# Kernel optimization log

Hardware: AMD Instinct MI355X
Metric: run time of the kernel (lower is better)

Reference implementation:

```python
import jax, jax.numpy as jnp
import numpy as np

NUM_MIX = 50
CMD_LEN = 4
ARG_LEN = 6
MIX_TEMP = 0.0001
GAUSS_TEMP = 0.0001


def setup_inputs() -> dict:
    key = jax.random.key(0)
    k1, k2, k3 = jax.random.split(key, 3)
    S, B, H = 51, 2048, 1024
    out_ch = CMD_LEN + ARG_LEN * NUM_MIX * 3  # 904
    decoder_output = jax.random.normal(k1, (S, B, H), dtype=jnp.float32)
    W = jax.random.normal(k2, (out_ch, H), dtype=jnp.float32) * (1.0 / np.sqrt(H))
    b = jax.random.normal(k3, (out_ch,), dtype=jnp.float32) * 0.01
    return {"decoder_output": decoder_output, "W": W, "b": b}


def reference(decoder_output, W, b):
    S, B, H = decoder_output.shape
    # fc: [S,B,H] @ [H,out_ch] + b  -> [S,B,904]
    ret = jnp.einsum('sbh,oh->sbo', decoder_output, W) + b

    key = jax.random.key(42)
    k_cmd, k_mix, k_gauss = jax.random.split(key, 3)

    # command: temperature softmax + categorical sample + one-hot
    cmd_logits = ret[..., :CMD_LEN] / MIX_TEMP  # [S,B,4]
    cmd_idx = jax.random.categorical(k_cmd, cmd_logits)  # [S,B]
    command = jax.nn.one_hot(cmd_idx, CMD_LEN, dtype=decoder_output.dtype)

    # MDN coefficients over flattened rows: N = S*B*ARG_LEN
    arguments = ret[..., CMD_LEN:].reshape(-1, 3 * NUM_MIX)  # [N,150]
    logmix = arguments[:, :NUM_MIX]
    mean = arguments[:, NUM_MIX:2 * NUM_MIX]
    logstd = arguments[:, 2 * NUM_MIX:]
    logmix = logmix - jax.nn.logsumexp(logmix, axis=-1, keepdims=True)

    # sample mixture component with temperature (softmax of logmix/temp)
    mix_idx = jax.random.categorical(k_mix, logmix / MIX_TEMP)  # [N]

    # vectorized gather of chosen mean/logstd (replaces per-row python loop)
    chosen_mean = jnp.take_along_axis(mean, mix_idx[:, None], axis=1)[:, 0]
    chosen_logstd = jnp.take_along_axis(logstd, mix_idx[:, None], axis=1)[:, 0]

    noise = jax.random.normal(k_gauss, chosen_mean.shape, dtype=chosen_mean.dtype)
    noise = noise * np.sqrt(GAUSS_TEMP)
    args_out = chosen_mean + jnp.exp(chosen_logstd) * noise  # [N]
    args_out = args_out.reshape(-1, B, ARG_LEN)  # [S,B,6]

    return jnp.concatenate([command, args_out], axis=-1)  # [S,B,10]
```

## Files before the change

### kernel.cpp

```cpp
#include <hip/hip_runtime.h>
#include <stdint.h>
#include <math.h>

#pragma clang fp contract(off)

#define M_TOTAL 104448
#define N_OUT   904
#define K_DIM   1024

#define BM 64
#define BN 64
#define BK 16

typedef float f32x2 __attribute__((ext_vector_type(2)));

__device__ inline f32x2 pk_mul(f32x2 a, f32x2 b) {
    f32x2 d;
    asm("v_pk_mul_f32 %0, %1, %2" : "=v"(d) : "v"(a), "v"(b));
    return d;
}
__device__ inline f32x2 pk_add(f32x2 a, f32x2 b) {
    f32x2 d;
    asm("v_pk_add_f32 %0, %1, %2" : "=v"(d) : "v"(a), "v"(b));
    return d;
}

__host__ __device__ inline uint32_t rotl32(uint32_t x, int r) {
    return (x << r) | (x >> (32 - r));
}

__host__ __device__ inline void threefry2x32(uint32_t k0, uint32_t k1,
                                             uint32_t x0, uint32_t x1,
                                             uint32_t& o0, uint32_t& o1) {
    uint32_t ks2 = k0 ^ k1 ^ 0x1BD11BDAu;
    x0 += k0; x1 += k1;
#define R4(a,b,c,d) \
    x0 += x1; x1 = rotl32(x1,(a)); x1 ^= x0; \
    x0 += x1; x1 = rotl32(x1,(b)); x1 ^= x0; \
    x0 += x1; x1 = rotl32(x1,(c)); x1 ^= x0; \
    x0 += x1; x1 = rotl32(x1,(d)); x1 ^= x0;
    R4(13,15,26,6)  x0 += k1;  x1 += ks2 + 1u;
    R4(17,29,16,24) x0 += ks2; x1 += k0  + 2u;
    R4(13,15,26,6)  x0 += k0;  x1 += k1  + 3u;
    R4(17,29,16,24) x0 += k1;  x1 += ks2 + 4u;
    R4(13,15,26,6)  x0 += ks2; x1 += k0  + 5u;
#undef R4
    o0 = x0; o1 = x1;
}

__device__ inline uint32_t random_bits_part(uint32_t k0, uint32_t k1, uint32_t idx) {
    uint32_t o0, o1;
    threefry2x32(k0, k1, 0u, idx, o0, o1);
    return o0 ^ o1;
}

__device__ inline float bits_to_unit(uint32_t bits) {
    return __uint_as_float((bits >> 9) | 0x3f800000u) - 1.0f;
}

__device__ inline float logf_cr(float x) { return (float)log((double)x); }
__device__ inline float expf_cr(float x) { return (float)exp((double)x); }

__device__ inline float gumbel_at(uint32_t k0, uint32_t k1, uint32_t idx) {
    float f = bits_to_unit(random_bits_part(k0, k1, idx));
    float u = fmaxf(f, 1.17549435e-38f);
    float t = logf_cr(u);
    return -logf_cr(-t);
}

__device__ inline float erfinv_xla(float x) {
    float w = -log1pf(-x * x);
    float p;
    if (w < 5.0f) {
        w = w - 2.5f;
        p = 2.81022636e-08f;
        p = 3.43273939e-07f  + p * w;
        p = -3.5233877e-06f  + p * w;
        p = -4.39150654e-06f + p * w;
        p = 0.00021858087f   + p * w;
        p = -0.00125372503f  + p * w;
        p = -0.00417768164f  + p * w;
        p = 0.246640727f     + p * w;
        p = 1.50140941f      + p * w;
    } else {
        w = sqrtf(w) - 3.0f;
        p = -0.000200214257f;
        p = 0.000100950558f  + p * w;
        p = 0.00134934322f   + p * w;
        p = -0.00367342844f  + p * w;
        p = 0.00573950773f   + p * w;
        p = -0.0076224613f   + p * w;
        p = 0.00943887047f   + p * w;
        p = 1.00167406f      + p * w;
        p = 2.83297682f      + p * w;
    }
    return p * x;
}

__global__ __launch_bounds__(256) void gemm_np_sse_pk2(
    const float* __restrict__ X,
    const float* __restrict__ W,
    const float* __restrict__ bias,
    float* __restrict__ ret,
    int rows)
{
    __shared__ f32x2 As2[8][68];
    __shared__ f32x2 Bs2[8][100];

    const int t  = threadIdx.x;
    const int tx = t & 15;
    const int ty = t >> 4;
    const int m0 = blockIdx.y * BM;
    const int n0 = blockIdx.x * BN;

    const int sm  = t >> 2;
    const int skq = t & 3;
    const int bse = sm + 2 * (sm >> 2);

    const float* Xrow = X + (size_t)(m0 + sm) * K_DIM + skq * 4;
    const float* Wrow = W + (size_t)(n0 + sm) * K_DIM + skq * 4;
    const bool   wok  = (n0 + sm) < N_OUT;

    f32x2 acc[2][4][4];
#pragma unroll
    for (int h = 0; h < 2; h++)
#pragma unroll
        for (int i = 0; i < 4; i++)
#pragma unroll
            for (int j = 0; j < 4; j++) acc[h][i][j] = (f32x2){0.0f, 0.0f};

    float4 av = *(const float4*)(Xrow);
    float4 bv = wok ? *(const float4*)(Wrow) : make_float4(0.f, 0.f, 0.f, 0.f);

    for (int k0 = 0; k0 < K_DIM; k0 += BK) {
        __syncthreads();
        As2[skq * 2 + 0][sm]  = (f32x2){av.x, av.y};
        As2[skq * 2 + 1][sm]  = (f32x2){av.z, av.w};
        Bs2[skq * 2 + 0][bse] = (f32x2){bv.x, bv.y};
        Bs2[skq * 2 + 1][bse] = (f32x2){bv.z, bv.w};
        __syncthreads();

        if (k0 + BK < K_DIM) {
            av = *(const float4*)(Xrow + k0 + BK);
            bv = wok ? *(const float4*)(Wrow + k0 + BK)
                     : make_float4(0.f, 0.f, 0.f, 0.f);
        }

#pragma unroll
        for (int q = 3; q >= 0; q--) {
#pragma unroll
            for (int h = 0; h < 2; h++) {
                const int kp = q * 2 + h;
                float4 aa0 = *(const float4*)&As2[kp][ty * 4];
                float4 aa1 = *(const float4*)&As2[kp][ty * 4 + 2];
                float4 bb0 = *(const float4*)&Bs2[kp][tx * 6];
                float4 bb1 = *(const float4*)&Bs2[kp][tx * 6 + 2];
                f32x2 a0 = {aa0.x, aa0.y}, a1 = {aa0.z, aa0.w};
                f32x2 a2 = {aa1.x, aa1.y}, a3 = {aa1.z, aa1.w};
                f32x2 b0 = {bb0.x, bb0.y}, b1 = {bb0.z, bb0.w};
                f32x2 b2 = {bb1.x, bb1.y}, b3 = {bb1.z, bb1.w};
                acc[h][0][0] = pk_add(pk_mul(a0, b0), acc[h][0][0]);
                acc[h][0][1] = pk_add(pk_mul(a0, b1), acc[h][0][1]);
                acc[h][0][2] = pk_add(pk_mul(a0, b2), acc[h][0][2]);
                acc[h][0][3] = pk_add(pk_mul(a0, b3), acc[h][0][3]);
                acc[h][1][0] = pk_add(pk_mul(a1, b0), acc[h][1][0]);
                acc[h][1][1] = pk_add(pk_mul(a1, b1), acc[h][1][1]);
                acc[h][1][2] = pk_add(pk_mul(a1, b2), acc[h][1][2]);
                acc[h][1][3] = pk_add(pk_mul(a1, b3), acc[h][1][3]);
                acc[h][2][0] = pk_add(pk_mul(a2, b0), acc[h][2][0]);
                acc[h][2][1] = pk_add(pk_mul(a2, b1), acc[h][2][1]);
                acc[h][2][2] = pk_add(pk_mul(a2, b2), acc[h][2][2]);
                acc[h][2][3] = pk_add(pk_mul(a2, b3), acc[h][2][3]);
                acc[h][3][0] = pk_add(pk_mul(a3, b0), acc[h][3][0]);
                acc[h][3][1] = pk_add(pk_mul(a3, b1), acc[h][3][1]);
                acc[h][3][2] = pk_add(pk_mul(a3, b2), acc[h][3][2]);
                acc[h][3][3] = pk_add(pk_mul(a3, b3), acc[h][3][3]);
            }
        }
    }

#pragma unroll
    for (int i = 0; i < 4; i++) {
        int m = m0 + ty * 4 + i;
        if (m >= rows) continue;
#pragma unroll
        for (int j = 0; j < 4; j++) {
            int o = n0 + tx * 4 + j;
            if (o >= N_OUT) continue;
            f32x2 s01 = acc[0][i][j];
            f32x2 s23 = acc[1][i][j];
            float res = (s01.x + s01.y) + (s23.x + s23.y);
            ret[(size_t)m * N_OUT + o] = res + bias[o];
        }
    }
}

__global__ __launch_bounds__(256) void sample_kernel(
    const float* __restrict__ ret,
    float* __restrict__ out,
    int m0_global, int rows,
    uint32_t kc0, uint32_t kc1,
    uint32_t km0, uint32_t km1,
    uint32_t kg0, uint32_t kg1)
{
    const int lane = threadIdx.x & 63;
    const int wid  = threadIdx.x >> 6;
    const int rloc = blockIdx.x * 4 + wid;
    if (rloc >= rows) return;
    const int m = m0_global + rloc;

    const float* r = ret + (size_t)rloc * N_OUT;
    float* o = out + (size_t)m * 10;

    const float LO = __uint_as_float(0xBF7FFFFFu);
    const float SQRT2 = __uint_as_float(0x3FB504F3u);

    {
        float v; int idx = lane;
        if (lane < 4) {
            float g = gumbel_at(kc0, kc1, (uint32_t)(m * 4 + lane));
            v = r[lane] / 0.0001f + g;
        } else {
            v = -INFINITY;
        }
#pragma unroll
        for (int off = 1; off < 64; off <<= 1) {
            float v2 = __shfl_xor(v, off);
            int   i2 = __shfl_xor(idx, off);
            if (v2 > v || (v2 == v && i2 < idx)) { v = v2; idx = i2; }
        }
        if (lane < 4) o[lane] = (lane == idx) ? 1.0f : 0.0f;
    }

    for (int a = 0; a < 6; a++) {
        const float* base = r + 4 + a * 150;
        float l = (lane < 50) ? base[lane] : -INFINITY;

        float mx = l;
#pragma unroll
        for (int off = 1; off < 64; off <<= 1) mx = fmaxf(mx, __shfl_xor(mx, off));

        float e = (lane < 50) ? expf_cr(l - mx) : 0.0f;

        float rj = (lane < 8) ? e : 0.0f;
#pragma unroll
        for (int tstep = 1; tstep <= 5; tstep++) {
            float ev = __shfl(e, (lane & 7) + 8 * tstep);
            if (lane < 8) rj = rj + ev;
        }
        float r0 = __shfl(rj, 0), r1 = __shfl(rj, 1), r2 = __shfl(rj, 2), r3 = __shfl(rj, 3);
        float r4 = __shfl(rj, 4), r5 = __shfl(rj, 5), r6 = __shfl(rj, 6), r7 = __shfl(rj, 7);
        float s = ((r0 + r1) + (r2 + r3)) + ((r4 + r5) + (r6 + r7));
        s = s + __shfl(e, 48);
        s = s + __shfl(e, 49);

        float lse = logf_cr(s) + mx;

        float vv; int ii = lane;
        if (lane < 50) {
            float g = gumbel_at(km0, km1, (uint32_t)((m * 6 + a) * 50 + lane));
            vv = (l - lse) / 0.0001f + g;
        } else {
            vv = -INFINITY;
        }
#pragma unroll
        for (int off = 1; off < 64; off <<= 1) {
            float v2 = __shfl_xor(vv, off);
            int   i2 = __shfl_xor(ii, off);
            if (v2 > vv || (v2 == vv && i2 < ii)) { vv = v2; ii = i2; }
        }

        if (lane == 0) {
            float mean = base[50 + ii];
            float lstd = base[100 + ii];
            uint32_t eidx = (uint32_t)(m * 6 + a);
            float f = bits_to_unit(random_bits_part(kg0, kg1, eidx));
            float val = f * 2.0f + LO;
            val = fmaxf(LO, val);
            float nrm = SQRT2 * erfinv_xla(val);
            float noise = nrm * 0.01f;
            o[4 + a] = mean + expf_cr(lstd) * noise;
        }
    }
}

extern "C" void kernel_launch(void* const* d_in, const int* in_sizes, int n_in,
                              void* d_out, int out_size, void* d_ws, size_t ws_size,
                              hipStream_t stream) {
    const float* X    = (const float*)d_in[0];
    const float* W    = (const float*)d_in[1];
    const float* bias = (const float*)d_in[2];
    float* out = (float*)d_out;
    float* ws  = (float*)d_ws;

    uint32_t kc0, kc1, km0, km1, kg0, kg1;
    threefry2x32(0u, 42u, 0u, 0u, kc0, kc1);
    threefry2x32(0u, 42u, 0u, 1u, km0, km1);
    threefry2x32(0u, 42u, 0u, 2u, kg0, kg1);

    const size_t rowBytes = (size_t)N_OUT * sizeof(float);
    size_t rowsCap = ws_size / rowBytes;
    int chunk = (rowsCap >= (size_t)M_TOTAL) ? M_TOTAL : (int)rowsCap;
    chunk -= chunk % BM;
    if (chunk <= 0) chunk = BM;

    const int gx = (N_OUT + BN - 1) / BN;

    for (int m0 = 0; m0 < M_TOTAL; m0 += chunk) {
        int rows = M_TOTAL - m0;
        if (rows > chunk) rows = chunk;
        dim3 ggrid(gx, rows / BM);
        gemm_np_sse_pk2<<<ggrid, 256, 0, stream>>>(X + (size_t)m0 * K_DIM, W, bias, ws, rows);
        sample_kernel<<<dim3(rows / 4), 256, 0, stream>>>(ws, out, m0, rows,
                                                          kc0, kc1, km0, km1, kg0, kg1);
    }
}
```

Measured before the change: 4.918 ms.

## Load A operand directly from global into registers, bypassing shared memory

```diff
diff --git a/kernel.cpp b/kernel.cpp
--- a/kernel.cpp
+++ b/kernel.cpp
@@ -97,14 +97,13 @@
     return p * x;
 }
 
-__global__ __launch_bounds__(256) void gemm_np_sse_pk2(
+__global__ __launch_bounds__(256) void gemm_np_sse_rAq(
     const float* __restrict__ X,
     const float* __restrict__ W,
     const float* __restrict__ bias,
     float* __restrict__ ret,
     int rows)
 {
-    __shared__ f32x2 As2[8][68];
     __shared__ f32x2 Bs2[8][100];
 
     const int t  = threadIdx.x;
@@ -113,13 +112,17 @@
     const int m0 = blockIdx.y * BM;
     const int n0 = blockIdx.x * BN;
 
-    const int sm  = t >> 2;
+    const int sn  = t >> 2;
     const int skq = t & 3;
-    const int bse = sm + 2 * (sm >> 2);
-
-    const float* Xrow = X + (size_t)(m0 + sm) * K_DIM + skq * 4;
-    const float* Wrow = W + (size_t)(n0 + sm) * K_DIM + skq * 4;
-    const bool   wok  = (n0 + sm) < N_OUT;
+    const int bse = sn + 2 * (sn >> 2);
+
+    const float* Wrow = W + (size_t)(n0 + sn) * K_DIM + skq * 4;
+    const bool   wok  = (n0 + sn) < N_OUT;
+
+    const float* Ar0 = X + (size_t)(m0 + ty * 4 + 0) * K_DIM;
+    const float* Ar1 = X + (size_t)(m0 + ty * 4 + 1) * K_DIM;
+    const float* Ar2 = X + (size_t)(m0 + ty * 4 + 2) * K_DIM;
+    const float* Ar3 = X + (size_t)(m0 + ty * 4 + 3) * K_DIM;
 
     f32x2 acc[2][4][4];
 #pragma unroll
@@ -129,55 +132,69 @@
 #pragma unroll
             for (int j = 0; j < 4; j++) acc[h][i][j] = (f32x2){0.0f, 0.0f};
 
-    float4 av = *(const float4*)(Xrow);
+    float4 A0[4], A1[4];
+
+#define LOADQ(BUF, KO)                                   \
+    do { const int _ko = (KO);                           \
+        BUF[0] = *(const float4*)(Ar0 + _ko);            \
+        BUF[1] = *(const float4*)(Ar1 + _ko);            \
+        BUF[2] = *(const float4*)(Ar2 + _ko);            \
+        BUF[3] = *(const float4*)(Ar3 + _ko);            \
+    } while (0)
+
+#define COMPUTE_Q(BUF, Q)                                                  \
+    do {                                                                   \
+        _Pragma("unroll")                                                  \
+        for (int h = 0; h < 2; h++) {                                      \
+            const int kp = (Q) * 2 + h;                                    \
+            float4 bb0 = *(const float4*)&Bs2[kp][tx * 6];                 \
+            float4 bb1 = *(const float4*)&Bs2[kp][tx * 6 + 2];             \
+            f32x2 b0 = {bb0.x, bb0.y}, b1 = {bb0.z, bb0.w};                \
+            f32x2 b2 = {bb1.x, bb1.y}, b3 = {bb1.z, bb1.w};                \
+            f32x2 a0 = h ? (f32x2){BUF[0].z, BUF[0].w} : (f32x2){BUF[0].x, BUF[0].y}; \
+            f32x2 a1 = h ? (f32x2){BUF[1].z, BUF[1].w} : (f32x2){BUF[1].x, BUF[1].y}; \
+            f32x2 a2 = h ? (f32x2){BUF[2].z, BUF[2].w} : (f32x2){BUF[2].x, BUF[2].y}; \
+            f32x2 a3 = h ? (f32x2){BUF[3].z, BUF[3].w} : (f32x2){BUF[3].x, BUF[3].y}; \
+            acc[h][0][0] = pk_add(pk_mul(a0, b0), acc[h][0][0]);           \
+            acc[h][0][1] = pk_add(pk_mul(a0, b1), acc[h][0][1]);           \
+            acc[h][0][2] = pk_add(pk_mul(a0, b2), acc[h][0][2]);           \
+            acc[h][0][3] = pk_add(pk_mul(a0, b3), acc[h][0][3]);           \
+            acc[h][1][0] = pk_add(pk_mul(a1, b0), acc[h][1][0]);           \
+            acc[h][1][1] = pk_add(pk_mul(a1, b1), acc[h][1][1]);           \
+            acc[h][1][2] = pk_add(pk_mul(a1, b2), acc[h][1][2]);           \
+            acc[h][1][3] = pk_add(pk_mul(a1, b3), acc[h][1][3]);           \
+            acc[h][2][0] = pk_add(pk_mul(a2, b0), acc[h][2][0]);           \
+            acc[h][2][1] = pk_add(pk_mul(a2, b1), acc[h][2][1]);           \
+            acc[h][2][2] = pk_add(pk_mul(a2, b2), acc[h][2][2]);           \
+            acc[h][2][3] = pk_add(pk_mul(a2, b3), acc[h][2][3]);           \
+            acc[h][3][0] = pk_add(pk_mul(a3, b0), acc[h][3][0]);           \
+            acc[h][3][1] = pk_add(pk_mul(a3, b1), acc[h][3][1]);           \
+            acc[h][3][2] = pk_add(pk_mul(a3, b2), acc[h][3][2]);           \
+            acc[h][3][3] = pk_add(pk_mul(a3, b3), acc[h][3][3]);           \
+        }                                                                  \
+    } while (0)
+
     float4 bv = wok ? *(const float4*)(Wrow) : make_float4(0.f, 0.f, 0.f, 0.f);
+    LOADQ(A0, 12);
 
     for (int k0 = 0; k0 < K_DIM; k0 += BK) {
         __syncthreads();
-        As2[skq * 2 + 0][sm]  = (f32x2){av.x, av.y};
-        As2[skq * 2 + 1][sm]  = (f32x2){av.z, av.w};
         Bs2[skq * 2 + 0][bse] = (f32x2){bv.x, bv.y};
         Bs2[skq * 2 + 1][bse] = (f32x2){bv.z, bv.w};
         __syncthreads();
 
-        if (k0 + BK < K_DIM) {
-            av = *(const float4*)(Xrow + k0 + BK);
+        if (k0 + BK < K_DIM)
             bv = wok ? *(const float4*)(Wrow + k0 + BK)
                      : make_float4(0.f, 0.f, 0.f, 0.f);
-        }
-
-#pragma unroll
-        for (int q = 3; q >= 0; q--) {
-#pragma unroll
-            for (int h = 0; h < 2; h++) {
-                const int kp = q * 2 + h;
-                float4 aa0 = *(const float4*)&As2[kp][ty * 4];
-                float4 aa1 = *(const float4*)&As2[kp][ty * 4 + 2];
-                float4 bb0 = *(const float4*)&Bs2[kp][tx * 6];
-                float4 bb1 = *(const float4*)&Bs2[kp][tx * 6 + 2];
-                f32x2 a0 = {aa0.x, aa0.y}, a1 = {aa0.z, aa0.w};
-                f32x2 a2 = {aa1.x, aa1.y}, a3 = {aa1.z, aa1.w};
-                f32x2 b0 = {bb0.x, bb0.y}, b1 = {bb0.z, bb0.w};
-                f32x2 b2 = {bb1.x, bb1.y}, b3 = {bb1.z, bb1.w};
-                acc[h][0][0] = pk_add(pk_mul(a0, b0), acc[h][0][0]);
-                acc[h][0][1] = pk_add(pk_mul(a0, b1), acc[h][0][1]);
-                acc[h][0][2] = pk_add(pk_mul(a0, b2), acc[h][0][2]);
-                acc[h][0][3] = pk_add(pk_mul(a0, b3), acc[h][0][3]);
-                acc[h][1][0] = pk_add(pk_mul(a1, b0), acc[h][1][0]);
-                acc[h][1][1] = pk_add(pk_mul(a1, b1), acc[h][1][1]);
-                acc[h][1][2] = pk_add(pk_mul(a1, b2), acc[h][1][2]);
-                acc[h][1][3] = pk_add(pk_mul(a1, b3), acc[h][1][3]);
-                acc[h][2][0] = pk_add(pk_mul(a2, b0), acc[h][2][0]);
-                acc[h][2][1] = pk_add(pk_mul(a2, b1), acc[h][2][1]);
-                acc[h][2][2] = pk_add(pk_mul(a2, b2), acc[h][2][2]);
-                acc[h][2][3] = pk_add(pk_mul(a2, b3), acc[h][2][3]);
-                acc[h][3][0] = pk_add(pk_mul(a3, b0), acc[h][3][0]);
-                acc[h][3][1] = pk_add(pk_mul(a3, b1), acc[h][3][1]);
-                acc[h][3][2] = pk_add(pk_mul(a3, b2), acc[h][3][2]);
-                acc[h][3][3] = pk_add(pk_mul(a3, b3), acc[h][3][3]);
-            }
-        }
-    }
+
+        COMPUTE_Q(A0, 3); LOADQ(A1, k0 + 8);
+        COMPUTE_Q(A1, 2); LOADQ(A0, k0 + 4);
+        COMPUTE_Q(A0, 1); LOADQ(A1, k0 + 0);
+        COMPUTE_Q(A1, 0);
+        if (k0 + BK < K_DIM) LOADQ(A0, k0 + BK + 12);
+    }
+#undef LOADQ
+#undef COMPUTE_Q
 
 #pragma unroll
     for (int i = 0; i < 4; i++) {
@@ -310,7 +327,7 @@
         int rows = M_TOTAL - m0;
         if (rows > chunk) rows = chunk;
         dim3 ggrid(gx, rows / BM);
-        gemm_np_sse_pk2<<<ggrid, 256, 0, stream>>>(X + (size_t)m0 * K_DIM, W, bias, ws, rows);
+        gemm_np_sse_rAq<<<ggrid, 256, 0, stream>>>(X + (size_t)m0 * K_DIM, W, bias, ws, rows);
         sample_kernel<<<dim3(rows / 4), 256, 0, stream>>>(ws, out, m0, rows,
                                                           kc0, kc1, km0, km1, kg0, kg1);
     }
```

After: 5.908 ms. 20.1% more time.
